# Kernel tuning notes

Hardware: AMD Instinct MI355X
Metric: run time of the kernel (lower is better)

Reference implementation:

```python
import jax, jax.numpy as jnp
import numpy as np

B, C, D = 8192, 1000, 2048
CLAMP_MIN, CLAMP_MAX = 1e-12, 1e12
SEP_WEIGHT = 0.001


def setup_inputs() -> dict:
    key = jax.random.key(0)
    k1, k2, k3 = jax.random.split(key, 3)
    x = jax.random.normal(k1, (B, D), dtype=jnp.float32)
    centers = jax.random.normal(k2, (C, D), dtype=jnp.float32)
    labels = jax.random.randint(k3, (B,), 0, C, dtype=jnp.int64)
    return {"x": x, "centers": centers, "labels": labels}


def reference(x, centers, labels):
    distmat = (
        jnp.sum(x * x, axis=1, keepdims=True)
        + jnp.sum(centers * centers, axis=1)[None, :]
        - 2.0 * (x @ centers.T)
    )
    d = jnp.clip(distmat, CLAMP_MIN, CLAMP_MAX)
    mask = labels[:, None] == jnp.arange(C, dtype=labels.dtype)[None, :]  # [B, C]
    bsz = x.shape[0]
    ncls = centers.shape[0]
    # each row has exactly one True in mask -> counts are B and B*(C-1)
    center_loss = jnp.sum(jnp.where(mask, d, 0.0)) / bsz
    sep_loss = jnp.sum(jnp.where(mask, 0.0, d)) / (bsz * (ncls - 1))
    return center_loss - SEP_WEIGHT * sep_loss
```

## Files before the change

kernel.cpp:

```cpp
#include <hip/hip_runtime.h>


#define DD 2048
#define NB 8192
#define NC 1000
#define D4 (DD / 4)
#define HALF4 256
#define THREADS 256
#define XROWS 8
#define XBLOCKS ((NB / XROWS) * 2)
#define CTILES 8
#define CRG 8
#define CBLOCKS (CTILES * CRG)

#define CQ_OFF   0
#define SC_OFF   65536
#define CSQ_OFF  73728
#define PART_OFF 73984

__device__ __forceinline__ float dot4(float4 a, float4 b) {
    return a.x * b.x + a.y * b.y + a.z * b.z + a.w * b.w;
}
__device__ __forceinline__ void acc4(float4& a, float4 b) {
    a.x += b.x; a.y += b.y; a.z += b.z; a.w += b.w;
}

__global__ __launch_bounds__(THREADS) void centers_kernel(
        const float4* __restrict__ c4, float4* __restrict__ cq,
        float* __restrict__ csq_part) {
    const int t = threadIdx.x;
    const int tile = blockIdx.x & (CTILES - 1);
    const int rg = blockIdx.x >> 3;
    const int col4 = tile * 64 + (t & 63);
    const int rlane = t >> 6;
    const int row0 = rg * 125;

    float4 acc = make_float4(0.f, 0.f, 0.f, 0.f);
    float csq = 0.f;
#pragma unroll 4
    for (int r = rlane; r < 125; r += 4) {
        float4 v = c4[(size_t)(row0 + r) * D4 + col4];
        acc4(acc, v);
        csq += dot4(v, v);
    }

    __shared__ float4 lds[4][64];
    lds[rlane][t & 63] = acc;
    __syncthreads();
    if (t < 64) {
        float4 s = lds[0][t];
        acc4(s, lds[1][t]); acc4(s, lds[2][t]); acc4(s, lds[3][t]);
        cq[rg * 512 + tile * 64 + t] = s;
    }

    __shared__ float red[THREADS / 64];
    for (int off = 32; off > 0; off >>= 1) csq += __shfl_down(csq, off, 64);
    const int lane = t & 63, wv = t >> 6;
    if (lane == 0) red[wv] = csq;
    __syncthreads();
    if (t == 0)
        csq_part[blockIdx.x] = red[0] + red[1] + red[2] + red[3];
}

__global__ __launch_bounds__(THREADS) void sc_fold_kernel(
        const float4* __restrict__ cq, float4* __restrict__ sc4) {
    const int idx = blockIdx.x * THREADS + threadIdx.x;
    float4 s = cq[idx];
#pragma unroll
    for (int r = 1; r < CRG; ++r) acc4(s, cq[r * 512 + idx]);
    sc4[idx] = s;
}

__global__ __launch_bounds__(THREADS) void x_kernel(
        const float4* __restrict__ x4, const float4* __restrict__ c4,
        const int* __restrict__ labels, const float4* __restrict__ sc4,
        float4* __restrict__ partials) {
    const int t = threadIdx.x;
    const int b = blockIdx.x;
    const int rowgrp = b >> 1;
    const int h = (b & 1) * HALF4;
    const int rows0 = rowgrp * XROWS;

    const float4* xr = x4 + (size_t)rows0 * D4 + h + t;
    const float4* cbase = c4 + h + t;

    const int4* l4 = (const int4*)(labels + rows0);
    const int4 la = l4[0], lb = l4[1];
    const int labs[XROWS] = {la.x, la.y, la.z, la.w, lb.x, lb.y, lb.z, lb.w};

    float4 xv[XROWS], cv[XROWS];
#pragma unroll
    for (int r = 0; r < XROWS; ++r) xv[r] = xr[(size_t)r * D4];
#pragma unroll
    for (int r = 0; r < XROWS; ++r) cv[r] = cbase[(size_t)labs[r] * D4];
    const float4 sc = sc4[h + t];

    float sx = 0.f, sdot = 0.f, scl = 0.f, s2 = 0.f;
#pragma unroll
    for (int r = 0; r < XROWS; ++r) {
        sx   += dot4(xv[r], xv[r]);
        sdot += dot4(xv[r], cv[r]);
        scl  += dot4(cv[r], cv[r]);
        s2   += dot4(xv[r], sc);
    }

    __shared__ float red[4][THREADS / 64];
    for (int off = 32; off > 0; off >>= 1) {
        sx   += __shfl_down(sx, off, 64);
        sdot += __shfl_down(sdot, off, 64);
        scl  += __shfl_down(scl, off, 64);
        s2   += __shfl_down(s2, off, 64);
    }
    const int lane = t & 63, wv = t >> 6;
    if (lane == 0) {
        red[0][wv] = sx; red[1][wv] = sdot;
        red[2][wv] = scl; red[3][wv] = s2;
    }
    __syncthreads();
    if (t == 0) {
        float4 s;
        s.x = red[0][0] + red[0][1] + red[0][2] + red[0][3];
        s.y = red[1][0] + red[1][1] + red[1][2] + red[1][3];
        s.z = red[2][0] + red[2][1] + red[2][2] + red[2][3];
        s.w = red[3][0] + red[3][1] + red[3][2] + red[3][3];
        partials[b] = s;
    }
}

__global__ __launch_bounds__(THREADS) void finalize_kernel(
        const float4* __restrict__ partials, const float* __restrict__ csq_part,
        float* __restrict__ out) {
    const int t = threadIdx.x;

    double sx = 0.0, sdot = 0.0, scl = 0.0, s2 = 0.0, csq = 0.0;
    for (int i = t; i < XBLOCKS; i += THREADS) {
        float4 p = partials[i];
        sx += (double)p.x; sdot += (double)p.y;
        scl += (double)p.z; s2 += (double)p.w;
    }
    if (t < CBLOCKS) csq = (double)csq_part[t];

    __shared__ double red[5][THREADS / 64];
    for (int off = 32; off > 0; off >>= 1) {
        sx   += __shfl_down(sx, off, 64);
        sdot += __shfl_down(sdot, off, 64);
        scl  += __shfl_down(scl, off, 64);
        s2   += __shfl_down(s2, off, 64);
        csq  += __shfl_down(csq, off, 64);
    }
    const int lane = t & 63, wv = t >> 6;
    if (lane == 0) {
        red[0][wv] = sx; red[1][wv] = sdot; red[2][wv] = scl;
        red[3][wv] = s2; red[4][wv] = csq;
    }
    __syncthreads();
    if (t == 0) {
        double Sx   = red[0][0] + red[0][1] + red[0][2] + red[0][3];
        double Sdot = red[1][0] + red[1][1] + red[1][2] + red[1][3];
        double Scl  = red[2][0] + red[2][1] + red[2][2] + red[2][3];
        double S2   = red[3][0] + red[3][1] + red[3][2] + red[3][3];
        double Sc   = red[4][0] + red[4][1] + red[4][2] + red[4][3];
        double sum_all  = (double)NC * Sx + (double)NB * Sc - 2.0 * S2;
        double sum_diag = Sx + Scl - 2.0 * Sdot;
        double center_loss = sum_diag / (double)NB;
        double sep_loss =
            (sum_all - sum_diag) / ((double)NB * (double)(NC - 1));
        out[0] = (float)(center_loss - 0.001 * sep_loss);
    }
}

extern "C" void kernel_launch(void* const* d_in, const int* in_sizes, int n_in,
                              void* d_out, int out_size, void* d_ws, size_t ws_size,
                              hipStream_t stream) {
    const float4* x4 = (const float4*)d_in[0];
    const float4* c4 = (const float4*)d_in[1];
    const int* labels = (const int*)d_in[2];

    float4* cq = (float4*)((char*)d_ws + CQ_OFF);
    float4* sc = (float4*)((char*)d_ws + SC_OFF);
    float* csq_part = (float*)((char*)d_ws + CSQ_OFF);
    float4* partials = (float4*)((char*)d_ws + PART_OFF);
    float* out = (float*)d_out;

    centers_kernel<<<CBLOCKS, THREADS, 0, stream>>>(c4, cq, csq_part);
    sc_fold_kernel<<<2, THREADS, 0, stream>>>((const float4*)cq, sc);
    x_kernel<<<XBLOCKS, THREADS, 0, stream>>>(x4, c4, labels,
                                              (const float4*)sc, partials);
    finalize_kernel<<<1, THREADS, 0, stream>>>(partials, csq_part, out);
}
```

Before: 111.9 us.

## Fuse centers and x passes into one kernel, defer x·sum(c) via column sums

Merges the centers reduction and the per-row x pass into a single launch, so the x pass no longer waits on the center column sum. Each x block now covers a full row width and writes per-block column sums of x, which a new fold kernel reduces; the cross term becomes a dot of the x and center column sums in finalize. Also adds nontemporal loads for x and software-prefetches the next row. The cost is an extra workspace round trip of about 8 MB of x partials and a 514-block fold kernel.

```diff
diff --git a/kernel.cpp b/kernel.cpp
--- a/kernel.cpp
+++ b/kernel.cpp
@@ -1,22 +1,26 @@
 #include <hip/hip_runtime.h>
 
+
+typedef float f32x4 __attribute__((ext_vector_type(4)));
 
 #define DD 2048
 #define NB 8192
 #define NC 1000
 #define D4 (DD / 4)
-#define HALF4 256
 #define THREADS 256
 #define XROWS 8
-#define XBLOCKS ((NB / XROWS) * 2)
+#define XBLK (NB / XROWS)
 #define CTILES 8
 #define CRG 8
 #define CBLOCKS (CTILES * CRG)
-
-#define CQ_OFF   0
-#define SC_OFF   65536
-#define CSQ_OFF  73728
-#define PART_OFF 73984
+#define GRID1 (CBLOCKS + XBLK)
+
+#define CQ_OFF    0
+#define SC_OFF    65536
+#define CSQ_OFF   73728
+#define PART_OFF  73984
+#define CSX_OFF   90368
+#define XPART_OFF 131072
 
 __device__ __forceinline__ float dot4(float4 a, float4 b) {
     return a.x * b.x + a.y * b.y + a.z * b.z + a.w * b.w;
@@ -24,121 +28,166 @@
 __device__ __forceinline__ void acc4(float4& a, float4 b) {
     a.x += b.x; a.y += b.y; a.z += b.z; a.w += b.w;
 }
-
-__global__ __launch_bounds__(THREADS) void centers_kernel(
-        const float4* __restrict__ c4, float4* __restrict__ cq,
-        float* __restrict__ csq_part) {
+__device__ __forceinline__ float4 ntload(const float4* p) {
+    f32x4 v = __builtin_nontemporal_load((const f32x4*)p);
+    return make_float4(v[0], v[1], v[2], v[3]);
+}
+
+__global__ __launch_bounds__(THREADS, 4) void main_kernel(
+        const float4* __restrict__ x4, const float4* __restrict__ c4,
+        const int* __restrict__ labels, float4* __restrict__ cq,
+        float* __restrict__ csq_part, float4* __restrict__ part,
+        float4* __restrict__ xpart) {
     const int t = threadIdx.x;
-    const int tile = blockIdx.x & (CTILES - 1);
-    const int rg = blockIdx.x >> 3;
-    const int col4 = tile * 64 + (t & 63);
-    const int rlane = t >> 6;
-    const int row0 = rg * 125;
-
-    float4 acc = make_float4(0.f, 0.f, 0.f, 0.f);
-    float csq = 0.f;
+
+    if (blockIdx.x < CBLOCKS) {
+        const int bid = blockIdx.x;
+        const int tile = bid & (CTILES - 1);
+        const int rg = bid >> 3;
+        const int col4 = tile * 64 + (t & 63);
+        const int rlane = t >> 6;
+        const int row0 = rg * 125;
+
+        float4 acc = make_float4(0.f, 0.f, 0.f, 0.f);
+        float csq = 0.f;
 #pragma unroll 4
-    for (int r = rlane; r < 125; r += 4) {
-        float4 v = c4[(size_t)(row0 + r) * D4 + col4];
-        acc4(acc, v);
-        csq += dot4(v, v);
-    }
-
-    __shared__ float4 lds[4][64];
-    lds[rlane][t & 63] = acc;
-    __syncthreads();
-    if (t < 64) {
-        float4 s = lds[0][t];
-        acc4(s, lds[1][t]); acc4(s, lds[2][t]); acc4(s, lds[3][t]);
-        cq[rg * 512 + tile * 64 + t] = s;
-    }
-
-    __shared__ float red[THREADS / 64];
-    for (int off = 32; off > 0; off >>= 1) csq += __shfl_down(csq, off, 64);
-    const int lane = t & 63, wv = t >> 6;
-    if (lane == 0) red[wv] = csq;
-    __syncthreads();
-    if (t == 0)
-        csq_part[blockIdx.x] = red[0] + red[1] + red[2] + red[3];
-}
-
-__global__ __launch_bounds__(THREADS) void sc_fold_kernel(
-        const float4* __restrict__ cq, float4* __restrict__ sc4) {
-    const int idx = blockIdx.x * THREADS + threadIdx.x;
-    float4 s = cq[idx];
-#pragma unroll
-    for (int r = 1; r < CRG; ++r) acc4(s, cq[r * 512 + idx]);
-    sc4[idx] = s;
-}
-
-__global__ __launch_bounds__(THREADS) void x_kernel(
-        const float4* __restrict__ x4, const float4* __restrict__ c4,
-        const int* __restrict__ labels, const float4* __restrict__ sc4,
-        float4* __restrict__ partials) {
-    const int t = threadIdx.x;
-    const int b = blockIdx.x;
-    const int rowgrp = b >> 1;
-    const int h = (b & 1) * HALF4;
-    const int rows0 = rowgrp * XROWS;
-
-    const float4* xr = x4 + (size_t)rows0 * D4 + h + t;
-    const float4* cbase = c4 + h + t;
+        for (int r = rlane; r < 125; r += 4) {
+            float4 v = c4[(size_t)(row0 + r) * D4 + col4];
+            acc4(acc, v);
+            csq += dot4(v, v);
+        }
+
+        __shared__ float4 lds[4][64];
+        lds[rlane][t & 63] = acc;
+        __syncthreads();
+        if (t < 64) {
+            float4 s = lds[0][t];
+            acc4(s, lds[1][t]); acc4(s, lds[2][t]); acc4(s, lds[3][t]);
+            cq[rg * 512 + tile * 64 + t] = s;
+        }
+
+        __shared__ float redc[THREADS / 64];
+        for (int off = 32; off > 0; off >>= 1)
+            csq += __shfl_down(csq, off, 64);
+        if ((t & 63) == 0) redc[t >> 6] = csq;
+        __syncthreads();
+        if (t == 0)
+            csq_part[bid] = redc[0] + redc[1] + redc[2] + redc[3];
+        return;
+    }
+
+    const int b = blockIdx.x - CBLOCKS;
+    const int rows0 = b * XROWS;
+
+    const float4* xr = x4 + (size_t)rows0 * D4 + t;
+    const float4* cb = c4 + t;
 
     const int4* l4 = (const int4*)(labels + rows0);
     const int4 la = l4[0], lb = l4[1];
     const int labs[XROWS] = {la.x, la.y, la.z, la.w, lb.x, lb.y, lb.z, lb.w};
 
-    float4 xv[XROWS], cv[XROWS];
-#pragma unroll
-    for (int r = 0; r < XROWS; ++r) xv[r] = xr[(size_t)r * D4];
-#pragma unroll
-    for (int r = 0; r < XROWS; ++r) cv[r] = cbase[(size_t)labs[r] * D4];
-    const float4 sc = sc4[h + t];
-
-    float sx = 0.f, sdot = 0.f, scl = 0.f, s2 = 0.f;
+    float sx = 0.f, sdot = 0.f, scl = 0.f;
+    float4 xs0 = make_float4(0.f, 0.f, 0.f, 0.f);
+    float4 xs1 = make_float4(0.f, 0.f, 0.f, 0.f);
+
+    float4 xa0 = ntload(xr);
+    float4 xa1 = ntload(xr + 256);
+    float4 ca0 = cb[(size_t)labs[0] * D4];
+    float4 ca1 = cb[(size_t)labs[0] * D4 + 256];
+
 #pragma unroll
     for (int r = 0; r < XROWS; ++r) {
-        sx   += dot4(xv[r], xv[r]);
-        sdot += dot4(xv[r], cv[r]);
-        scl  += dot4(cv[r], cv[r]);
-        s2   += dot4(xv[r], sc);
-    }
-
-    __shared__ float red[4][THREADS / 64];
+        float4 nx0, nx1, nc0, nc1;
+        if (r + 1 < XROWS) {
+            const size_t xo = (size_t)(r + 1) * D4;
+            const size_t co = (size_t)labs[r + 1] * D4;
+            nx0 = ntload(xr + xo);
+            nx1 = ntload(xr + xo + 256);
+            nc0 = cb[co];
+            nc1 = cb[co + 256];
+        }
+        sx   += dot4(xa0, xa0) + dot4(xa1, xa1);
+        sdot += dot4(xa0, ca0) + dot4(xa1, ca1);
+        scl  += dot4(ca0, ca0) + dot4(ca1, ca1);
+        acc4(xs0, xa0);
+        acc4(xs1, xa1);
+        if (r + 1 < XROWS) { xa0 = nx0; xa1 = nx1; ca0 = nc0; ca1 = nc1; }
+    }
+
+    xpart[(size_t)b * D4 + t] = xs0;
+    xpart[(size_t)b * D4 + 256 + t] = xs1;
+
+    __shared__ float red[3][THREADS / 64];
     for (int off = 32; off > 0; off >>= 1) {
         sx   += __shfl_down(sx, off, 64);
         sdot += __shfl_down(sdot, off, 64);
         scl  += __shfl_down(scl, off, 64);
-        s2   += __shfl_down(s2, off, 64);
     }
     const int lane = t & 63, wv = t >> 6;
-    if (lane == 0) {
-        red[0][wv] = sx; red[1][wv] = sdot;
-        red[2][wv] = scl; red[3][wv] = s2;
-    }
+    if (lane == 0) { red[0][wv] = sx; red[1][wv] = sdot; red[2][wv] = scl; }
     __syncthreads();
     if (t == 0) {
         float4 s;
         s.x = red[0][0] + red[0][1] + red[0][2] + red[0][3];
         s.y = red[1][0] + red[1][1] + red[1][2] + red[1][3];
         s.z = red[2][0] + red[2][1] + red[2][2] + red[2][3];
-        s.w = red[3][0] + red[3][1] + red[3][2] + red[3][3];
-        partials[b] = s;
+        s.w = 0.f;
+        part[b] = s;
+    }
+}
+
+__global__ __launch_bounds__(THREADS) void fold_kernel(
+        const float4* __restrict__ xpart, const float4* __restrict__ cq,
+        float4* __restrict__ csx, float4* __restrict__ sc4) {
+    const int t = threadIdx.x;
+    const int j = blockIdx.x;
+
+    if (j < 512) {
+        float4 a = make_float4(0.f, 0.f, 0.f, 0.f);
+#pragma unroll
+        for (int m = 0; m < 4; ++m)
+            acc4(a, xpart[(size_t)(t + 256 * m) * D4 + j]);
+
+        __shared__ float4 red[THREADS / 64];
+        for (int off = 32; off > 0; off >>= 1) {
+            a.x += __shfl_down(a.x, off, 64);
+            a.y += __shfl_down(a.y, off, 64);
+            a.z += __shfl_down(a.z, off, 64);
+            a.w += __shfl_down(a.w, off, 64);
+        }
+        if ((t & 63) == 0) red[t >> 6] = a;
+        __syncthreads();
+        if (t == 0) {
+            float4 s = red[0];
+            acc4(s, red[1]); acc4(s, red[2]); acc4(s, red[3]);
+            csx[j] = s;
+        }
+    } else {
+        const int idx = (j - 512) * THREADS + t;
+        float4 s = cq[idx];
+#pragma unroll
+        for (int r = 1; r < CRG; ++r) acc4(s, cq[r * 512 + idx]);
+        sc4[idx] = s;
     }
 }
 
 __global__ __launch_bounds__(THREADS) void finalize_kernel(
-        const float4* __restrict__ partials, const float* __restrict__ csq_part,
+        const float4* __restrict__ part, const float* __restrict__ csq_part,
+        const float4* __restrict__ csx, const float4* __restrict__ sc4,
         float* __restrict__ out) {
     const int t = threadIdx.x;
 
     double sx = 0.0, sdot = 0.0, scl = 0.0, s2 = 0.0, csq = 0.0;
-    for (int i = t; i < XBLOCKS; i += THREADS) {
-        float4 p = partials[i];
-        sx += (double)p.x; sdot += (double)p.y;
-        scl += (double)p.z; s2 += (double)p.w;
+    for (int i = t; i < XBLK; i += THREADS) {
+        float4 p = part[i];
+        sx += (double)p.x; sdot += (double)p.y; scl += (double)p.z;
     }
     if (t < CBLOCKS) csq = (double)csq_part[t];
+    for (int c = t; c < 512; c += THREADS) {
+        float4 a = csx[c], s = sc4[c];
+        s2 += (double)a.x * s.x + (double)a.y * s.y
+            + (double)a.z * s.z + (double)a.w * s.w;
+    }
 
     __shared__ double red[5][THREADS / 64];
     for (int off = 32; off > 0; off >>= 1) {
@@ -179,12 +228,16 @@
     float4* cq = (float4*)((char*)d_ws + CQ_OFF);
     float4* sc = (float4*)((char*)d_ws + SC_OFF);
     float* csq_part = (float*)((char*)d_ws + CSQ_OFF);
-    float4* partials = (float4*)((char*)d_ws + PART_OFF);
+    float4* part = (float4*)((char*)d_ws + PART_OFF);
+    float4* csx = (float4*)((char*)d_ws + CSX_OFF);
+    float4* xpart = (float4*)((char*)d_ws + XPART_OFF);
     float* out = (float*)d_out;
 
-    centers_kernel<<<CBLOCKS, THREADS, 0, stream>>>(c4, cq, csq_part);
-    sc_fold_kernel<<<2, THREADS, 0, stream>>>((const float4*)cq, sc);
-    x_kernel<<<XBLOCKS, THREADS, 0, stream>>>(x4, c4, labels,
-                                              (const float4*)sc, partials);
-    finalize_kernel<<<1, THREADS, 0, stream>>>(partials, csq_part, out);
-}
+    main_kernel<<<GRID1, THREADS, 0, stream>>>(x4, c4, labels, cq,
+                                               csq_part, part, xpart);
+    fold_kernel<<<514, THREADS, 0, stream>>>((const float4*)xpart,
+                                             (const float4*)cq, csx, sc);
+    finalize_kernel<<<1, THREADS, 0, stream>>>((const float4*)part, csq_part,
+                                               (const float4*)csx,
+                                               (const float4*)sc, out);
+}
```

Result: slower. 124.8 us (+11.5%).
